# Performance work log

Hardware: AMD Instinct MI355X
Metric: run time of the kernel (lower is better)

Reference implementation:

```python
import jax, jax.numpy as jnp
import numpy as np

NS, NV = 32, 8                      # scalar / vector multiplicities
N_NODES, N_EDGES, N_EF = 10000, 100000, 64
W1, W2, W3, W4 = NS*NS, NV*NV, NS*NV, NV*NS   # path weight sizes
WNUM = W1 + W2 + W3 + W4            # 1600
D_NODE = NS + 3*NV                  # 56

def mish(x):
    return x * jnp.tanh(jax.nn.softplus(x))

def setup_inputs() -> dict:
    key = jax.random.key(0)
    ks = jax.random.split(key, 8)
    return dict(
        node_attr=jax.random.normal(ks[0], (N_NODES, D_NODE), jnp.float32),
        edge_index=jax.random.randint(ks[1], (2, N_EDGES), 0, N_NODES),
        edge_attr=jax.random.normal(ks[2], (N_EDGES, N_EF), jnp.float32),
        edge_sh=jax.random.normal(ks[3], (N_EDGES, 4), jnp.float32),
        fc1_w=jax.random.normal(ks[4], (N_EF, N_EF), jnp.float32) / np.sqrt(N_EF),
        fc1_b=jnp.zeros((N_EF,), jnp.float32),
        fc2_w=jax.random.normal(ks[5], (N_EF, WNUM), jnp.float32) / np.sqrt(N_EF),
        fc2_b=jnp.zeros((WNUM,), jnp.float32),
        bn_gamma_s=jnp.ones((NS,), jnp.float32),
        bn_beta_s=jnp.zeros((NS,), jnp.float32),
        bn_gamma_v=jnp.ones((NV,), jnp.float32),
    )

def reference(node_attr, edge_index, edge_attr, edge_sh,
              fc1_w, fc1_b, fc2_w, fc2_b,
              bn_gamma_s, bn_beta_s, bn_gamma_v):
    edge_src, edge_dst = edge_index[0], edge_index[1]
    # edge-conditioned TP weights: Linear -> Mish -> Linear
    w = mish(edge_attr @ fc1_w + fc1_b) @ fc2_w + fc2_b            # [E, WNUM]
    w1 = w[:, :W1].reshape(-1, NS, NS)           # 0e x 0e -> 0e
    w2 = w[:, W1:W1+W2].reshape(-1, NV, NV)      # 1o x 0e -> 1o
    w3 = w[:, W1+W2:W1+W2+W3].reshape(-1, NS, NV)  # 0e x 1o -> 1o
    w4 = w[:, W1+W2+W3:].reshape(-1, NV, NS)     # 1o x 1o -> 0e
    # gather destination node features
    x = node_attr[edge_dst]
    s = x[:, :NS]                                # [E,NS]
    v = x[:, NS:].reshape(-1, NV, 3)             # [E,NV,3]
    sh0 = edge_sh[:, 0]                          # [E]
    sh1 = edge_sh[:, 1:4]                        # [E,3]
    # path normalization: 1/sqrt(total fan-in per output irrep) = 1/sqrt(NS+NV)
    a = 1.0 / np.sqrt(float(NS + NV))
    dot = jnp.einsum('euc,ec->eu', v, sh1) / np.sqrt(3.0)  # CG(1,1,0)
    out_s = a * (jnp.einsum('eu,euw->ew', s * sh0[:, None], w1)
               + jnp.einsum('eu,euw->ew', dot, w4))          # [E,NS]
    out_v = a * (jnp.einsum('euc,euw->ewc', v * sh0[:, None, None], w2)
               + jnp.einsum('eu,ec,euw->ewc', s, sh1, w3))   # [E,NV,3]
    tp = jnp.concatenate([out_s, out_v.reshape(-1, 3*NV)], axis=-1)  # [E,D_NODE]
    # scatter-mean over edge_src
    summ = jax.ops.segment_sum(tp, edge_src, num_segments=N_NODES)
    cnt = jax.ops.segment_sum(jnp.ones((N_EDGES,), tp.dtype), edge_src, num_segments=N_NODES)
    out = summ / jnp.maximum(cnt, 1.0)[:, None]
    # residual (in/out irreps equal -> pad is a no-op)
    out = out + node_attr
    # e3nn-style BatchNorm (training batch stats), eps=1e-4, component norm
    eps = 1e-4
    os = out[:, :NS]
    ov = out[:, NS:].reshape(-1, NV, 3)
    mu = os.mean(axis=0)
    osc = os - mu
    var = (osc * osc).mean(axis=0)
    os_n = osc * jax.lax.rsqrt(var + eps) * bn_gamma_s + bn_beta_s
    vn = (ov * ov).mean(axis=-1).mean(axis=0)                 # [NV]
    ov_n = ov * (jax.lax.rsqrt(vn + eps) * bn_gamma_v)[None, :, None]
    return jnp.concatenate([os_n, ov_n.reshape(-1, 3*NV)], axis=-1)
```

## Files before the change

### kernel.cpp

```cpp
#include <hip/hip_runtime.h>
#include <stdint.h>

#define NNODES 10000
#define NEDGES 100000
#define DNODE 56
#define JTOT 1600

typedef __attribute__((ext_vector_type(8))) short short8;
typedef __attribute__((ext_vector_type(4))) float floatx4;

__device__ __forceinline__ unsigned short f2bf(float f) {
  unsigned u = __float_as_uint(f);
  u = u + 0x7fffu + ((u >> 16) & 1u);
  return (unsigned short)(u >> 16);
}

__device__ __forceinline__ float mishf(float x) {
  float e = __expf(x);
  float z = 1.f + e; z = z * z;
  float t = (z - 1.f) / (z + 1.f);
  t = (x > 40.f) ? 1.f : t;
  return x * t;
}

__global__ __launch_bounds__(256) void k_tr(const float* __restrict__ fc2w,
                                            unsigned short* __restrict__ G) {
  int idx = blockIdx.x * 256 + threadIdx.x;
  if (idx >= 64 * JTOT) return;
  int j = idx >> 6, k = idx & 63;
  G[idx] = f2bf(fc2w[k * JTOT + j]);
}

__global__ __launch_bounds__(256) void k_hidden(const float* __restrict__ ea,
                                                const float* __restrict__ fc1w,
                                                const float* __restrict__ fc1b,
                                                const int* __restrict__ eidx,
                                                int* __restrict__ cntn,
                                                unsigned short* __restrict__ hb) {
  int e = blockIdx.x * 256 + threadIdx.x;
  if (e >= NEDGES) return;
  atomicAdd(&cntn[eidx[e]], 1);
  float a[64];
  const float4* row = (const float4*)(ea + (size_t)e * 64);
  #pragma unroll
  for (int i = 0; i < 16; i++) {
    float4 t = row[i];
    a[4*i] = t.x; a[4*i+1] = t.y; a[4*i+2] = t.z; a[4*i+3] = t.w;
  }
  for (int jb = 0; jb < 64; jb += 8) {
    float acc[8];
    #pragma unroll
    for (int i = 0; i < 8; i++) acc[i] = fc1b[jb + i];
    #pragma unroll
    for (int k = 0; k < 64; k++) {
      #pragma unroll
      for (int i = 0; i < 8; i++) acc[i] = fmaf(a[k], fc1w[k*64 + jb + i], acc[i]);
    }
    unsigned pk[4];
    #pragma unroll
    for (int i = 0; i < 4; i++) {
      unsigned lo = f2bf(mishf(acc[2*i]));
      unsigned hi = f2bf(mishf(acc[2*i+1]));
      pk[i] = lo | (hi << 16);
    }
    *(uint4*)(hb + (size_t)e*64 + jb) = make_uint4(pk[0], pk[1], pk[2], pk[3]);
  }
}

__global__ __launch_bounds__(1024) void k_scan(const int* __restrict__ cntn,
                                               int* __restrict__ offs,
                                               int* __restrict__ cursor) {
  __shared__ int ts[1024];
  int t = threadIdx.x;
  int base = t * 10;
  int loc[10]; int s = 0;
  #pragma unroll
  for (int i = 0; i < 10; i++) {
    int idx = base + i;
    int v = (idx < NNODES) ? cntn[idx] : 0;
    loc[i] = s; s += v;
  }
  ts[t] = s;
  __syncthreads();
  for (int off = 1; off < 1024; off <<= 1) {
    int v = (t >= off) ? ts[t - off] : 0;
    __syncthreads();
    ts[t] += v;
    __syncthreads();
  }
  int excl = (t == 0) ? 0 : ts[t - 1];
  #pragma unroll
  for (int i = 0; i < 10; i++) {
    int idx = base + i;
    if (idx < NNODES) { int o = excl + loc[i]; offs[idx] = o; cursor[idx] = o; }
  }
  if (t == 1023) offs[NNODES] = ts[1023];
}

__global__ __launch_bounds__(256) void k_perm(const int* __restrict__ eidx,
                                              int* __restrict__ cursor,
                                              int* __restrict__ pos) {
  int e = blockIdx.x * 256 + threadIdx.x;
  if (e >= NEDGES) return;
  pos[e] = atomicAdd(&cursor[eidx[e]], 1);
}

__global__ __launch_bounds__(256, 2) void k_tp(
    const unsigned short* __restrict__ hb,
    const unsigned short* __restrict__ G,
    const float* __restrict__ fc2b,
    const int* __restrict__ eidx,
    const float* __restrict__ node_attr,
    const float* __restrict__ edge_sh,
    const int* __restrict__ pos,
    float* __restrict__ tp) {
  __shared__ float b2s[JTOT];
  __shared__ float X[2][64 * 64];
  __shared__ int pos_s[2][64];
  const int tid = threadIdx.x;
  const int wave = tid >> 6, lane = tid & 63;
  const int eg = wave & 1, jh = wave >> 1;
  for (int i = tid; i < JTOT; i += 256) b2s[i] = fc2b[i];

  const int e0 = (blockIdx.x * 2 + eg) * 64;
  float* Wt = &X[eg][0];
  if (jh == 0) {
    int e = e0 + lane;
    bool valid = e < NEDGES;
    int dst = valid ? eidx[NEDGES + e] : 0;
    pos_s[eg][lane] = valid ? pos[e] : 0;
    float4 sh = valid ? *(const float4*)(edge_sh + 4*(size_t)e) : make_float4(0.f,0.f,0.f,0.f);
    const float* na = node_attr + (size_t)dst * DNODE;
    #pragma unroll
    for (int u = 0; u < 32; u += 4) {
      float4 t = *(const float4*)(na + u);
      Wt[(u+0)*64 + lane] = t.x;
      Wt[(u+1)*64 + lane] = t.y;
      Wt[(u+2)*64 + lane] = t.z;
      Wt[(u+3)*64 + lane] = t.w;
    }
    const float rs3 = 0.57735026918962576f;
    #pragma unroll
    for (int u = 0; u < 8; u++) {
      float v0 = na[32 + u*3 + 0];
      float v1 = na[32 + u*3 + 1];
      float v2 = na[32 + u*3 + 2];
      Wt[(32 + u*3 + 0)*64 + lane] = v0;
      Wt[(32 + u*3 + 1)*64 + lane] = v1;
      Wt[(32 + u*3 + 2)*64 + lane] = v2;
      Wt[(56 + u)*64 + lane] = (v0*sh.y + v1*sh.z + v2*sh.w) * rs3;
    }
  }
  __syncthreads();

  const int col = lane & 15, rg = lane >> 4, rgh = rg >> 1;
  float sh0c[4], sh1c[4][3];
  bool vld[4];
  short8 bfrag[4][2];
  const short8 zfrag = {0,0,0,0,0,0,0,0};
  #pragma unroll
  for (int nt = 0; nt < 4; nt++) {
    int e = e0 + nt*16 + col;
    bool v = e < NEDGES; vld[nt] = v;
    if (v) {
      float4 sh = *(const float4*)(edge_sh + 4*(size_t)e);
      sh0c[nt] = sh.x; sh1c[nt][0] = sh.y; sh1c[nt][1] = sh.z; sh1c[nt][2] = sh.w;
      const unsigned short* hp = hb + (size_t)e * 64;
      bfrag[nt][0] = *(const short8*)(hp + rg*8);
      bfrag[nt][1] = *(const short8*)(hp + 32 + rg*8);
    } else {
      sh0c[nt] = 0.f; sh1c[nt][0] = sh1c[nt][1] = sh1c[nt][2] = 0.f;
      bfrag[nt][0] = zfrag; bfrag[nt][1] = zfrag;
    }
  }

  float sacc[4][8], vacc[4][12];
  #pragma unroll
  for (int nt = 0; nt < 4; nt++) {
    #pragma unroll
    for (int i = 0; i < 8; i++) sacc[nt][i] = 0.f;
    #pragma unroll
    for (int i = 0; i < 12; i++) vacc[nt][i] = 0.f;
  }

  auto ldpair = [&](int p, short8& f0, short8& f1, short8& f2, short8& f3) {
    const unsigned short* q0 = G + ((((2*p) << 4) + col) << 6) + rg*8;
    f0 = *(const short8*)q0;
    f1 = *(const short8*)(q0 + 32);
    const unsigned short* q1 = q0 + 1024;
    f2 = *(const short8*)q1;
    f3 = *(const short8*)(q1 + 32);
  };

  short8 cur0, cur1, cur2, cur3, nx0, nx1, nx2, nx3;
  ldpair(jh, cur0, cur1, cur2, cur3);

  #pragma unroll 1
  for (int pp = 0; pp < 25; pp++) {
    const int p = 2*pp + jh;
    const int pn = (pp < 24) ? (p + 2) : p;
    ldpair(pn, nx0, nx1, nx2, nx3);
    const int jt0 = 2*p;
    float4 bb0 = *(const float4*)&b2s[jt0*16 + rg*4];
    float4 bb1 = *(const float4*)&b2s[(jt0+1)*16 + rg*4];
    floatx4 acc0[4], acc1[4];
    #pragma unroll
    for (int nt = 0; nt < 4; nt++) {
      floatx4 c0 = {bb0.x, bb0.y, bb0.z, bb0.w};
      c0 = __builtin_amdgcn_mfma_f32_16x16x32_bf16(cur0, bfrag[nt][0], c0, 0, 0, 0);
      c0 = __builtin_amdgcn_mfma_f32_16x16x32_bf16(cur1, bfrag[nt][1], c0, 0, 0, 0);
      acc0[nt] = c0;
      floatx4 c1 = {bb1.x, bb1.y, bb1.z, bb1.w};
      c1 = __builtin_amdgcn_mfma_f32_16x16x32_bf16(cur2, bfrag[nt][0], c1, 0, 0, 0);
      c1 = __builtin_amdgcn_mfma_f32_16x16x32_bf16(cur3, bfrag[nt][1], c1, 0, 0, 0);
      acc1[nt] = c1;
    }
    if (p < 32) {
      #pragma unroll
      for (int nt = 0; nt < 4; nt++) {
        float cf = Wt[p*64 + nt*16 + col] * sh0c[nt];
        #pragma unroll
        for (int r = 0; r < 4; r++) {
          sacc[nt][r]   = fmaf(cf, acc0[nt][r], sacc[nt][r]);
          sacc[nt][4+r] = fmaf(cf, acc1[nt][r], sacc[nt][4+r]);
        }
      }
    } else if (p < 34) {
      const int u0 = (jt0 - 64)*2 + rgh, u1 = u0 + 2;
      #pragma unroll
      for (int nt = 0; nt < 4; nt++) {
        #pragma unroll
        for (int c3 = 0; c3 < 3; c3++) {
          float cf0 = Wt[(32 + u0*3 + c3)*64 + nt*16 + col] * sh0c[nt];
          float cf1 = Wt[(32 + u1*3 + c3)*64 + nt*16 + col] * sh0c[nt];
          #pragma unroll
          for (int r = 0; r < 4; r++) {
            vacc[nt][c3*4+r] = fmaf(cf0, acc0[nt][r], vacc[nt][c3*4+r]);
            vacc[nt][c3*4+r] = fmaf(cf1, acc1[nt][r], vacc[nt][c3*4+r]);
          }
        }
      }
    } else if (p < 42) {
      const int u0 = (jt0 - 68)*2 + rgh, u1 = u0 + 2;
      #pragma unroll
      for (int nt = 0; nt < 4; nt++) {
        float sv0 = Wt[u0*64 + nt*16 + col];
        float sv1 = Wt[u1*64 + nt*16 + col];
        #pragma unroll
        for (int c3 = 0; c3 < 3; c3++) {
          float cf0 = sv0 * sh1c[nt][c3];
          float cf1 = sv1 * sh1c[nt][c3];
          #pragma unroll
          for (int r = 0; r < 4; r++) {
            vacc[nt][c3*4+r] = fmaf(cf0, acc0[nt][r], vacc[nt][c3*4+r]);
            vacc[nt][c3*4+r] = fmaf(cf1, acc1[nt][r], vacc[nt][c3*4+r]);
          }
        }
      }
    } else {
      const int u = p - 42;
      #pragma unroll
      for (int nt = 0; nt < 4; nt++) {
        float cf = Wt[(56 + u)*64 + nt*16 + col];
        #pragma unroll
        for (int r = 0; r < 4; r++) {
          sacc[nt][r]   = fmaf(cf, acc0[nt][r], sacc[nt][r]);
          sacc[nt][4+r] = fmaf(cf, acc1[nt][r], sacc[nt][4+r]);
        }
      }
    }
    cur0 = nx0; cur1 = nx1; cur2 = nx2; cur3 = nx3;
  }

  __syncthreads();
  if (jh == 1) {
    #pragma unroll
    for (int nt = 0; nt < 4; nt++)
      #pragma unroll
      for (int k = 0; k < 8; k++)
        Wt[(nt*8 + k)*64 + lane] = sacc[nt][k];
    #pragma unroll
    for (int nt = 0; nt < 4; nt++)
      #pragma unroll
      for (int k = 0; k < 12; k++) {
        float tot = vacc[nt][k] + __shfl_xor(vacc[nt][k], 32);
        if (rg < 2) Wt[2048 + (nt*12 + k)*32 + lane] = tot;
      }
  }
  __syncthreads();
  if (jh == 0) {
    const float ascale = 0.15811388300841897f;
    #pragma unroll
    for (int nt = 0; nt < 4; nt++)
      #pragma unroll
      for (int k = 0; k < 8; k++)
        sacc[nt][k] = (sacc[nt][k] + Wt[(nt*8 + k)*64 + lane]) * ascale;
    float vtot[4][12];
    #pragma unroll
    for (int nt = 0; nt < 4; nt++)
      #pragma unroll
      for (int k = 0; k < 12; k++) {
        float t0 = vacc[nt][k] + __shfl_xor(vacc[nt][k], 32);
        vtot[nt][k] = (t0 + Wt[2048 + (nt*12 + k)*32 + (lane & 31)]) * ascale;
      }
    #pragma unroll
    for (int nt = 0; nt < 4; nt++) {
      int el = nt*16 + col;
      #pragma unroll
      for (int pq = 0; pq < 2; pq++) {
        int q = pq*4 + rg;
        *(float4*)&Wt[el*64 + (((q + el) & 15) << 2)] = *(float4*)&sacc[nt][pq*4];
      }
      if (rg < 2) {
        float tmp[12];
        #pragma unroll
        for (int c3 = 0; c3 < 3; c3++)
          #pragma unroll
          for (int r = 0; r < 4; r++) tmp[r*3 + c3] = vtot[nt][c3*4 + r];
        #pragma unroll
        for (int j = 0; j < 3; j++) {
          int q = 8 + rg*3 + j;
          *(float4*)&Wt[el*64 + (((q + el) & 15) << 2)] = *(float4*)&tmp[j*4];
        }
      }
    }
    #pragma unroll
    for (int it = 0; it < 14; it++) {
      int flat = it*64 + lane;
      int el = flat / 14, fq = flat - el*14;
      int e = e0 + el;
      if (e < NEDGES) {
        float4 val = *(const float4*)&Wt[el*64 + (((fq + el) & 15) << 2)];
        *(float4*)(tp + (size_t)pos_s[eg][el]*DNODE + fq*4) = val;
      }
    }
  }
}

__global__ __launch_bounds__(256) void k_gather(const float* __restrict__ tp,
                                                const int* __restrict__ offs,
                                                const float* __restrict__ node_attr,
                                                float* __restrict__ pre,
                                                float* __restrict__ pstat) {
  __shared__ float redS[4*64], redQ[4*64];
  int t = threadIdx.x, wave = t >> 6, lane = t & 63;
  int gw = blockIdx.x * 4 + wave;
  const int W = 640 * 4;
  int off = (lane < DNODE) ? lane : 0;
  float ssum = 0.f, ssq = 0.f;
  for (int n = gw; n < NNODES; n += W) {
    int beg = offs[n], end = offs[n+1];
    float acc = 0.f;
    int i = beg;
    for (; i + 4 <= end; i += 4) {
      float v0 = tp[(size_t)(i+0)*DNODE + off];
      float v1 = tp[(size_t)(i+1)*DNODE + off];
      float v2 = tp[(size_t)(i+2)*DNODE + off];
      float v3 = tp[(size_t)(i+3)*DNODE + off];
      acc += (v0 + v1) + (v2 + v3);
    }
    for (; i < end; i++) acc += tp[(size_t)i*DNODE + off];
    int c = end - beg; if (c < 1) c = 1;
    float m = acc / (float)c + node_attr[(size_t)n*DNODE + off];
    if (lane < DNODE) { pre[(size_t)n*DNODE + lane] = m; ssum += m; ssq += m*m; }
  }
  redS[wave*64 + lane] = ssum;
  redQ[wave*64 + lane] = ssq;
  __syncthreads();
  if (wave == 0 && lane < DNODE) {
    float a = redS[lane] + redS[64+lane] + redS[128+lane] + redS[192+lane];
    float b = redQ[lane] + redQ[64+lane] + redQ[128+lane] + redQ[192+lane];
    pstat[(size_t)blockIdx.x*112 + lane] = a;
    pstat[(size_t)blockIdx.x*112 + 56 + lane] = b;
  }
}

__global__ __launch_bounds__(256) void k_stats(const float* __restrict__ pstat,
                                               float* __restrict__ stats) {
  int f = blockIdx.x * 4 + (threadIdx.x >> 6);
  int lane = threadIdx.x & 63;
  float v = 0.f;
  for (int b = lane; b < 640; b += 64) v += pstat[(size_t)b*112 + f];
  #pragma unroll
  for (int o = 32; o; o >>= 1) v += __shfl_xor(v, o);
  if (lane == 0) stats[f] = v;
}

__global__ __launch_bounds__(256) void k_norm(const float* __restrict__ pre,
                                              const float* __restrict__ stats,
                                              const float* __restrict__ gs,
                                              const float* __restrict__ bs,
                                              const float* __restrict__ gv,
                                              float* __restrict__ out) {
  int idx = blockIdx.x * 256 + threadIdx.x;
  if (idx >= NNODES * DNODE) return;
  int n = idx / DNODE;
  int d = idx - n * DNODE;
  float val = pre[idx];
  const float invN = 1.f / (float)NNODES;
  float res;
  if (d < 32) {
    float mu = stats[d] * invN;
    float var = stats[56 + d] * invN - mu * mu;
    res = (val - mu) * rsqrtf(var + 1e-4f) * gs[d] + bs[d];
  } else {
    int wi = (d - 32) / 3;
    float vn = (stats[56 + 32 + wi*3] + stats[56 + 32 + wi*3 + 1] +
                stats[56 + 32 + wi*3 + 2]) * (invN / 3.f);
    res = val * rsqrtf(vn + 1e-4f) * gv[wi];
  }
  out[idx] = res;
}

extern "C" void kernel_launch(void* const* d_in, const int* in_sizes, int n_in,
                              void* d_out, int out_size, void* d_ws, size_t ws_size,
                              hipStream_t stream) {
  const float* node_attr = (const float*)d_in[0];
  const int*   eidx      = (const int*)d_in[1];
  const float* edge_attr = (const float*)d_in[2];
  const float* edge_sh   = (const float*)d_in[3];
  const float* fc1w      = (const float*)d_in[4];
  const float* fc1b      = (const float*)d_in[5];
  const float* fc2w      = (const float*)d_in[6];
  const float* fc2b      = (const float*)d_in[7];
  const float* gs        = (const float*)d_in[8];
  const float* bs        = (const float*)d_in[9];
  const float* gv        = (const float*)d_in[10];

  float* ws = (float*)d_ws;
  float* tp    = ws;
  float* pre   = ws + 5600000;
  float* stats = ws + 6160000;
  float* pstat = ws + 6160128;
  int*   cntn  = (int*)(ws + 6231808);
  int*   offs  = (int*)(ws + 6241808);
  int*   cursor= (int*)(ws + 6251816);
  int*   pos   = (int*)(ws + 6261816);
  unsigned short* G  = (unsigned short*)(ws + 6361816);
  unsigned short* hb = (unsigned short*)(ws + 6413016);

  hipMemsetAsync(cntn, 0, (size_t)10000 * 4, stream);
  k_tr<<<400, 256, 0, stream>>>(fc2w, G);
  k_hidden<<<(NEDGES + 255) / 256, 256, 0, stream>>>(edge_attr, fc1w, fc1b, eidx, cntn, hb);
  k_scan<<<1, 1024, 0, stream>>>(cntn, offs, cursor);
  k_perm<<<(NEDGES + 255) / 256, 256, 0, stream>>>(eidx, cursor, pos);
  k_tp<<<782, 256, 0, stream>>>(hb, G, fc2b, eidx, node_attr, edge_sh, pos, tp);
  k_gather<<<640, 256, 0, stream>>>(tp, offs, node_attr, pre, pstat);
  k_stats<<<28, 256, 0, stream>>>(pstat, stats);
  k_norm<<<(NNODES * DNODE + 255) / 256, 256, 0, stream>>>(pre, stats, gs, bs, gv, (float*)d_out);
}
```

Measured before the change: 239.8 us.

## Restructure TP kernel: per-wave edges, LDS-staged weights, fused perm and transpose kernels

Merges the fc2 weight transpose into the hidden-layer kernel and folds the permutation atomics into the TP kernel, removing two launches and the pos buffer. The TP kernel now gives each wave 32 edges across all 1600 weight columns instead of splitting columns between waves. The shared bf16 weight matrix is staged through double-buffered, swizzled LDS by the whole block instead of each wave loading it from global memory. It also drops the cross-wave reduction and the LDS transpose before the output write, and raises occupancy to 3 blocks per SM. The trade-offs are a __syncthreads in every one of the 50 chunk iterations and uncoalesced direct output stores.

```diff
diff --git a/kernel.cpp b/kernel.cpp
--- a/kernel.cpp
+++ b/kernel.cpp
@@ -5,6 +5,8 @@
 #define NEDGES 100000
 #define DNODE 56
 #define JTOT 1600
+#define HBLK 391
+#define TBLK 400
 
 typedef __attribute__((ext_vector_type(8))) short short8;
 typedef __attribute__((ext_vector_type(4))) float floatx4;
@@ -23,21 +25,24 @@
   return x * t;
 }
 
-__global__ __launch_bounds__(256) void k_tr(const float* __restrict__ fc2w,
-                                            unsigned short* __restrict__ G) {
-  int idx = blockIdx.x * 256 + threadIdx.x;
-  if (idx >= 64 * JTOT) return;
-  int j = idx >> 6, k = idx & 63;
-  G[idx] = f2bf(fc2w[k * JTOT + j]);
-}
-
-__global__ __launch_bounds__(256) void k_hidden(const float* __restrict__ ea,
-                                                const float* __restrict__ fc1w,
-                                                const float* __restrict__ fc1b,
-                                                const int* __restrict__ eidx,
-                                                int* __restrict__ cntn,
-                                                unsigned short* __restrict__ hb) {
-  int e = blockIdx.x * 256 + threadIdx.x;
+__global__ __launch_bounds__(256) void k_hidtr(const float* __restrict__ ea,
+                                               const float* __restrict__ fc1w,
+                                               const float* __restrict__ fc1b,
+                                               const float* __restrict__ fc2w,
+                                               const int* __restrict__ eidx,
+                                               int* __restrict__ cntn,
+                                               unsigned short* __restrict__ hb,
+                                               unsigned short* __restrict__ G) {
+  int bid = blockIdx.x;
+  if (bid >= HBLK) {
+    int idx = (bid - HBLK) * 256 + threadIdx.x;
+    if (idx < 64 * JTOT) {
+      int j = idx >> 6, k = idx & 63;
+      G[idx] = f2bf(fc2w[k * JTOT + j]);
+    }
+    return;
+  }
+  int e = bid * 256 + threadIdx.x;
   if (e >= NEDGES) return;
   atomicAdd(&cntn[eidx[e]], 1);
   float a[64];
@@ -97,70 +102,65 @@
   if (t == 1023) offs[NNODES] = ts[1023];
 }
 
-__global__ __launch_bounds__(256) void k_perm(const int* __restrict__ eidx,
-                                              int* __restrict__ cursor,
-                                              int* __restrict__ pos) {
-  int e = blockIdx.x * 256 + threadIdx.x;
-  if (e >= NEDGES) return;
-  pos[e] = atomicAdd(&cursor[eidx[e]], 1);
-}
-
-__global__ __launch_bounds__(256, 2) void k_tp(
+__global__ __launch_bounds__(256, 3) void k_tp(
     const unsigned short* __restrict__ hb,
     const unsigned short* __restrict__ G,
     const float* __restrict__ fc2b,
     const int* __restrict__ eidx,
     const float* __restrict__ node_attr,
     const float* __restrict__ edge_sh,
-    const int* __restrict__ pos,
+    int* __restrict__ cursor,
     float* __restrict__ tp) {
+  __shared__ short Gs[2][2][1024];
   __shared__ float b2s[JTOT];
-  __shared__ float X[2][64 * 64];
-  __shared__ int pos_s[2][64];
+  __shared__ float Wt4[4][64 * 32];
+  __shared__ int pos_s[4][32];
   const int tid = threadIdx.x;
   const int wave = tid >> 6, lane = tid & 63;
-  const int eg = wave & 1, jh = wave >> 1;
   for (int i = tid; i < JTOT; i += 256) b2s[i] = fc2b[i];
 
-  const int e0 = (blockIdx.x * 2 + eg) * 64;
-  float* Wt = &X[eg][0];
-  if (jh == 0) {
-    int e = e0 + lane;
+  const int e0w = blockIdx.x * 128 + wave * 32;
+  float* Wt = &Wt4[wave][0];
+  {
+    int el = lane & 31, hh = lane >> 5;
+    int e = e0w + el;
     bool valid = e < NEDGES;
     int dst = valid ? eidx[NEDGES + e] : 0;
-    pos_s[eg][lane] = valid ? pos[e] : 0;
-    float4 sh = valid ? *(const float4*)(edge_sh + 4*(size_t)e) : make_float4(0.f,0.f,0.f,0.f);
     const float* na = node_attr + (size_t)dst * DNODE;
-    #pragma unroll
-    for (int u = 0; u < 32; u += 4) {
-      float4 t = *(const float4*)(na + u);
-      Wt[(u+0)*64 + lane] = t.x;
-      Wt[(u+1)*64 + lane] = t.y;
-      Wt[(u+2)*64 + lane] = t.z;
-      Wt[(u+3)*64 + lane] = t.w;
-    }
-    const float rs3 = 0.57735026918962576f;
-    #pragma unroll
-    for (int u = 0; u < 8; u++) {
-      float v0 = na[32 + u*3 + 0];
-      float v1 = na[32 + u*3 + 1];
-      float v2 = na[32 + u*3 + 2];
-      Wt[(32 + u*3 + 0)*64 + lane] = v0;
-      Wt[(32 + u*3 + 1)*64 + lane] = v1;
-      Wt[(32 + u*3 + 2)*64 + lane] = v2;
-      Wt[(56 + u)*64 + lane] = (v0*sh.y + v1*sh.z + v2*sh.w) * rs3;
-    }
-  }
-  __syncthreads();
+    if (hh == 0) {
+      pos_s[wave][el] = valid ? atomicAdd(&cursor[eidx[e]], 1) : 0;
+      #pragma unroll
+      for (int u = 0; u < 32; u += 4) {
+        float4 t = valid ? *(const float4*)(na + u) : make_float4(0.f,0.f,0.f,0.f);
+        Wt[(u+0)*32 + el] = t.x;
+        Wt[(u+1)*32 + el] = t.y;
+        Wt[(u+2)*32 + el] = t.z;
+        Wt[(u+3)*32 + el] = t.w;
+      }
+    } else {
+      float4 sh = valid ? *(const float4*)(edge_sh + 4*(size_t)e) : make_float4(0.f,0.f,0.f,0.f);
+      const float rs3 = 0.57735026918962576f;
+      #pragma unroll
+      for (int u = 0; u < 8; u++) {
+        float v0 = valid ? na[32 + u*3 + 0] : 0.f;
+        float v1 = valid ? na[32 + u*3 + 1] : 0.f;
+        float v2 = valid ? na[32 + u*3 + 2] : 0.f;
+        Wt[(32 + u*3 + 0)*32 + el] = v0;
+        Wt[(32 + u*3 + 1)*32 + el] = v1;
+        Wt[(32 + u*3 + 2)*32 + el] = v2;
+        Wt[(56 + u)*32 + el] = (v0*sh.y + v1*sh.z + v2*sh.w) * rs3;
+      }
+    }
+  }
 
   const int col = lane & 15, rg = lane >> 4, rgh = rg >> 1;
-  float sh0c[4], sh1c[4][3];
-  bool vld[4];
-  short8 bfrag[4][2];
+  float sh0c[2], sh1c[2][3];
+  bool vld[2];
+  short8 bfrag[2][2];
   const short8 zfrag = {0,0,0,0,0,0,0,0};
   #pragma unroll
-  for (int nt = 0; nt < 4; nt++) {
-    int e = e0 + nt*16 + col;
+  for (int nt = 0; nt < 2; nt++) {
+    int e = e0w + nt*16 + col;
     bool v = e < NEDGES; vld[nt] = v;
     if (v) {
       float4 sh = *(const float4*)(edge_sh + 4*(size_t)e);
@@ -174,165 +174,121 @@
     }
   }
 
-  float sacc[4][8], vacc[4][12];
-  #pragma unroll
-  for (int nt = 0; nt < 4; nt++) {
+  float sacc[2][8], vacc[2][12];
+  #pragma unroll
+  for (int nt = 0; nt < 2; nt++) {
     #pragma unroll
     for (int i = 0; i < 8; i++) sacc[nt][i] = 0.f;
     #pragma unroll
     for (int i = 0; i < 12; i++) vacc[nt][i] = 0.f;
   }
 
-  auto ldpair = [&](int p, short8& f0, short8& f1, short8& f2, short8& f3) {
-    const unsigned short* q0 = G + ((((2*p) << 4) + col) << 6) + rg*8;
-    f0 = *(const short8*)q0;
-    f1 = *(const short8*)(q0 + 32);
-    const unsigned short* q1 = q0 + 1024;
-    f2 = *(const short8*)q1;
-    f3 = *(const short8*)(q1 + 32);
+  auto stage = [&](int c) {
+    int t = tid >> 7, gt = tid & 127;
+    int jp = gt >> 3, g = gt & 7;
+    int gsw = (gt & ~7) | (g ^ (jp & 7));
+    short8 v = *(const short8*)(G + (size_t)c*2048 + tid*8);
+    *(short8*)(&Gs[c&1][t][gsw*8]) = v;
   };
 
-  short8 cur0, cur1, cur2, cur3, nx0, nx1, nx2, nx3;
-  ldpair(jh, cur0, cur1, cur2, cur3);
+  const int g0 = (rg ^ (col & 7)) * 8;
+  const int g1 = ((rg + 4) ^ (col & 7)) * 8;
+
+  stage(0);
+  __syncthreads();
 
   #pragma unroll 1
-  for (int pp = 0; pp < 25; pp++) {
-    const int p = 2*pp + jh;
-    const int pn = (pp < 24) ? (p + 2) : p;
-    ldpair(pn, nx0, nx1, nx2, nx3);
-    const int jt0 = 2*p;
-    float4 bb0 = *(const float4*)&b2s[jt0*16 + rg*4];
-    float4 bb1 = *(const float4*)&b2s[(jt0+1)*16 + rg*4];
-    floatx4 acc0[4], acc1[4];
-    #pragma unroll
-    for (int nt = 0; nt < 4; nt++) {
-      floatx4 c0 = {bb0.x, bb0.y, bb0.z, bb0.w};
-      c0 = __builtin_amdgcn_mfma_f32_16x16x32_bf16(cur0, bfrag[nt][0], c0, 0, 0, 0);
-      c0 = __builtin_amdgcn_mfma_f32_16x16x32_bf16(cur1, bfrag[nt][1], c0, 0, 0, 0);
-      acc0[nt] = c0;
-      floatx4 c1 = {bb1.x, bb1.y, bb1.z, bb1.w};
-      c1 = __builtin_amdgcn_mfma_f32_16x16x32_bf16(cur2, bfrag[nt][0], c1, 0, 0, 0);
-      c1 = __builtin_amdgcn_mfma_f32_16x16x32_bf16(cur3, bfrag[nt][1], c1, 0, 0, 0);
-      acc1[nt] = c1;
-    }
-    if (p < 32) {
-      #pragma unroll
-      for (int nt = 0; nt < 4; nt++) {
-        float cf = Wt[p*64 + nt*16 + col] * sh0c[nt];
+  for (int c = 0; c < 50; c++) {
+    if (c < 49) stage(c + 1);
+    #pragma unroll
+    for (int t = 0; t < 2; t++) {
+      const int jt = c*2 + t;
+      const short* gb = &Gs[c&1][t][0];
+      short8 x0 = *(const short8*)(gb + col*64 + g0);
+      short8 x1 = *(const short8*)(gb + col*64 + g1);
+      float4 bb = *(const float4*)&b2s[jt*16 + rg*4];
+      floatx4 acc[2];
+      #pragma unroll
+      for (int nt = 0; nt < 2; nt++) {
+        floatx4 cc = {bb.x, bb.y, bb.z, bb.w};
+        cc = __builtin_amdgcn_mfma_f32_16x16x32_bf16(x0, bfrag[nt][0], cc, 0, 0, 0);
+        cc = __builtin_amdgcn_mfma_f32_16x16x32_bf16(x1, bfrag[nt][1], cc, 0, 0, 0);
+        acc[nt] = cc;
+      }
+      if (jt < 64) {
+        const int u = jt >> 1, p = jt & 1;
         #pragma unroll
-        for (int r = 0; r < 4; r++) {
-          sacc[nt][r]   = fmaf(cf, acc0[nt][r], sacc[nt][r]);
-          sacc[nt][4+r] = fmaf(cf, acc1[nt][r], sacc[nt][4+r]);
+        for (int nt = 0; nt < 2; nt++) {
+          float cf = Wt[u*32 + nt*16 + col] * sh0c[nt];
+          #pragma unroll
+          for (int r = 0; r < 4; r++)
+            sacc[nt][p*4+r] = fmaf(cf, acc[nt][r], sacc[nt][p*4+r]);
+        }
+      } else if (jt < 68) {
+        const int u = (jt - 64)*2 + rgh;
+        #pragma unroll
+        for (int nt = 0; nt < 2; nt++) {
+          #pragma unroll
+          for (int c3 = 0; c3 < 3; c3++) {
+            float cf = Wt[(32 + u*3 + c3)*32 + nt*16 + col] * sh0c[nt];
+            #pragma unroll
+            for (int r = 0; r < 4; r++)
+              vacc[nt][c3*4+r] = fmaf(cf, acc[nt][r], vacc[nt][c3*4+r]);
+          }
+        }
+      } else if (jt < 84) {
+        const int u = (jt - 68)*2 + rgh;
+        #pragma unroll
+        for (int nt = 0; nt < 2; nt++) {
+          float sv = Wt[u*32 + nt*16 + col];
+          #pragma unroll
+          for (int c3 = 0; c3 < 3; c3++) {
+            float cf = sv * sh1c[nt][c3];
+            #pragma unroll
+            for (int r = 0; r < 4; r++)
+              vacc[nt][c3*4+r] = fmaf(cf, acc[nt][r], vacc[nt][c3*4+r]);
+          }
+        }
+      } else {
+        const int u = (jt - 84) >> 1, p = jt & 1;
+        #pragma unroll
+        for (int nt = 0; nt < 2; nt++) {
+          float cf = Wt[(56 + u)*32 + nt*16 + col];
+          #pragma unroll
+          for (int r = 0; r < 4; r++)
+            sacc[nt][p*4+r] = fmaf(cf, acc[nt][r], sacc[nt][p*4+r]);
         }
       }
-    } else if (p < 34) {
-      const int u0 = (jt0 - 64)*2 + rgh, u1 = u0 + 2;
-      #pragma unroll
-      for (int nt = 0; nt < 4; nt++) {
+    }
+    __syncthreads();
+  }
+
+  const float ascale = 0.15811388300841897f;
+  #pragma unroll
+  for (int nt = 0; nt < 2; nt++) {
+    int el = nt*16 + col;
+    float* rowp = tp + (size_t)pos_s[wave][el] * DNODE;
+    if (vld[nt]) {
+      #pragma unroll
+      for (int p = 0; p < 2; p++) {
+        float4 v = make_float4(ascale*sacc[nt][p*4+0], ascale*sacc[nt][p*4+1],
+                               ascale*sacc[nt][p*4+2], ascale*sacc[nt][p*4+3]);
+        *(float4*)(rowp + p*16 + rg*4) = v;
+      }
+    }
+    float vtot[12];
+    #pragma unroll
+    for (int k = 0; k < 12; k++)
+      vtot[k] = (vacc[nt][k] + __shfl_xor(vacc[nt][k], 32)) * ascale;
+    if (rg < 2 && vld[nt]) {
+      float tmp[12];
+      #pragma unroll
+      for (int c3 = 0; c3 < 3; c3++)
         #pragma unroll
-        for (int c3 = 0; c3 < 3; c3++) {
-          float cf0 = Wt[(32 + u0*3 + c3)*64 + nt*16 + col] * sh0c[nt];
-          float cf1 = Wt[(32 + u1*3 + c3)*64 + nt*16 + col] * sh0c[nt];
-          #pragma unroll
-          for (int r = 0; r < 4; r++) {
-            vacc[nt][c3*4+r] = fmaf(cf0, acc0[nt][r], vacc[nt][c3*4+r]);
-            vacc[nt][c3*4+r] = fmaf(cf1, acc1[nt][r], vacc[nt][c3*4+r]);
-          }
-        }
-      }
-    } else if (p < 42) {
-      const int u0 = (jt0 - 68)*2 + rgh, u1 = u0 + 2;
-      #pragma unroll
-      for (int nt = 0; nt < 4; nt++) {
-        float sv0 = Wt[u0*64 + nt*16 + col];
-        float sv1 = Wt[u1*64 + nt*16 + col];
-        #pragma unroll
-        for (int c3 = 0; c3 < 3; c3++) {
-          float cf0 = sv0 * sh1c[nt][c3];
-          float cf1 = sv1 * sh1c[nt][c3];
-          #pragma unroll
-          for (int r = 0; r < 4; r++) {
-            vacc[nt][c3*4+r] = fmaf(cf0, acc0[nt][r], vacc[nt][c3*4+r]);
-            vacc[nt][c3*4+r] = fmaf(cf1, acc1[nt][r], vacc[nt][c3*4+r]);
-          }
-        }
-      }
-    } else {
-      const int u = p - 42;
-      #pragma unroll
-      for (int nt = 0; nt < 4; nt++) {
-        float cf = Wt[(56 + u)*64 + nt*16 + col];
-        #pragma unroll
-        for (int r = 0; r < 4; r++) {
-          sacc[nt][r]   = fmaf(cf, acc0[nt][r], sacc[nt][r]);
-          sacc[nt][4+r] = fmaf(cf, acc1[nt][r], sacc[nt][4+r]);
-        }
-      }
-    }
-    cur0 = nx0; cur1 = nx1; cur2 = nx2; cur3 = nx3;
-  }
-
-  __syncthreads();
-  if (jh == 1) {
-    #pragma unroll
-    for (int nt = 0; nt < 4; nt++)
-      #pragma unroll
-      for (int k = 0; k < 8; k++)
-        Wt[(nt*8 + k)*64 + lane] = sacc[nt][k];
-    #pragma unroll
-    for (int nt = 0; nt < 4; nt++)
-      #pragma unroll
-      for (int k = 0; k < 12; k++) {
-        float tot = vacc[nt][k] + __shfl_xor(vacc[nt][k], 32);
-        if (rg < 2) Wt[2048 + (nt*12 + k)*32 + lane] = tot;
-      }
-  }
-  __syncthreads();
-  if (jh == 0) {
-    const float ascale = 0.15811388300841897f;
-    #pragma unroll
-    for (int nt = 0; nt < 4; nt++)
-      #pragma unroll
-      for (int k = 0; k < 8; k++)
-        sacc[nt][k] = (sacc[nt][k] + Wt[(nt*8 + k)*64 + lane]) * ascale;
-    float vtot[4][12];
-    #pragma unroll
-    for (int nt = 0; nt < 4; nt++)
-      #pragma unroll
-      for (int k = 0; k < 12; k++) {
-        float t0 = vacc[nt][k] + __shfl_xor(vacc[nt][k], 32);
-        vtot[nt][k] = (t0 + Wt[2048 + (nt*12 + k)*32 + (lane & 31)]) * ascale;
-      }
-    #pragma unroll
-    for (int nt = 0; nt < 4; nt++) {
-      int el = nt*16 + col;
-      #pragma unroll
-      for (int pq = 0; pq < 2; pq++) {
-        int q = pq*4 + rg;
-        *(float4*)&Wt[el*64 + (((q + el) & 15) << 2)] = *(float4*)&sacc[nt][pq*4];
-      }
-      if (rg < 2) {
-        float tmp[12];
-        #pragma unroll
-        for (int c3 = 0; c3 < 3; c3++)
-          #pragma unroll
-          for (int r = 0; r < 4; r++) tmp[r*3 + c3] = vtot[nt][c3*4 + r];
-        #pragma unroll
-        for (int j = 0; j < 3; j++) {
-          int q = 8 + rg*3 + j;
-          *(float4*)&Wt[el*64 + (((q + el) & 15) << 2)] = *(float4*)&tmp[j*4];
-        }
-      }
-    }
-    #pragma unroll
-    for (int it = 0; it < 14; it++) {
-      int flat = it*64 + lane;
-      int el = flat / 14, fq = flat - el*14;
-      int e = e0 + el;
-      if (e < NEDGES) {
-        float4 val = *(const float4*)&Wt[el*64 + (((fq + el) & 15) << 2)];
-        *(float4*)(tp + (size_t)pos_s[eg][el]*DNODE + fq*4) = val;
-      }
+        for (int r = 0; r < 4; r++) tmp[r*3 + c3] = vtot[c3*4 + r];
+      #pragma unroll
+      for (int j = 0; j < 3; j++)
+        *(float4*)(rowp + 32 + (rg & 1)*12 + j*4) = *(float4*)&tmp[j*4];
     }
   }
 }
@@ -435,16 +391,13 @@
   int*   cntn  = (int*)(ws + 6231808);
   int*   offs  = (int*)(ws + 6241808);
   int*   cursor= (int*)(ws + 6251816);
-  int*   pos   = (int*)(ws + 6261816);
-  unsigned short* G  = (unsigned short*)(ws + 6361816);
-  unsigned short* hb = (unsigned short*)(ws + 6413016);
+  unsigned short* G  = (unsigned short*)(ws + 6261816);
+  unsigned short* hb = (unsigned short*)(ws + 6313016);
 
   hipMemsetAsync(cntn, 0, (size_t)10000 * 4, stream);
-  k_tr<<<400, 256, 0, stream>>>(fc2w, G);
-  k_hidden<<<(NEDGES + 255) / 256, 256, 0, stream>>>(edge_attr, fc1w, fc1b, eidx, cntn, hb);
+  k_hidtr<<<HBLK + TBLK, 256, 0, stream>>>(edge_attr, fc1w, fc1b, fc2w, eidx, cntn, hb, G);
   k_scan<<<1, 1024, 0, stream>>>(cntn, offs, cursor);
-  k_perm<<<(NEDGES + 255) / 256, 256, 0, stream>>>(eidx, cursor, pos);
-  k_tp<<<782, 256, 0, stream>>>(hb, G, fc2b, eidx, node_attr, edge_sh, pos, tp);
+  k_tp<<<782, 256, 0, stream>>>(hb, G, fc2b, eidx, node_attr, edge_sh, cursor, tp);
   k_gather<<<640, 256, 0, stream>>>(tp, offs, node_attr, pre, pstat);
   k_stats<<<28, 256, 0, stream>>>(pstat, stats);
   k_norm<<<(NNODES * DNODE + 255) / 256, 256, 0, stream>>>(pre, stats, gs, bs, gv, (float*)d_out);
```

New measurement: 241.3 us. Within noise of the previous version (+0.6%).
